# Kernel optimization log

Measured on AMD Instinct MI355X. Metric: run time of the kernel, lower is better.

## Reference

```python
import jax, jax.numpy as jnp
import numpy as np

N_CLASSES = 512


def setup_inputs() -> dict:
    key = jax.random.key(0)
    k1, k2 = jax.random.split(key)
    x0 = jax.random.normal(k1, (16, 8192, 1, 128), dtype=jnp.float32)
    # nn.Parameter(torch.randn(n_channels, n_classes, vec_len) * 0.001)
    embedding0 = jax.random.normal(k2, (1, N_CLASSES, 128), dtype=jnp.float32) * 0.001
    return {"x0": x0, "embedding0": embedding0}


def reference(x0, embedding0):
    # normalize=False path: x = x0, embedding = embedding0
    x = x0
    embedding = embedding0
    B, S, C, L = x.shape
    K = embedding.shape[1]
    xf = x.reshape(B * S, C, L)

    x2 = jnp.sum(xf * xf, axis=-1)                      # (BS, C)
    e2 = jnp.sum(embedding * embedding, axis=-1)        # (C, K)
    dot = jnp.einsum('bcl,ckl->bck', xf, embedding)     # (BS, C, K)
    d2 = x2[:, :, None] - 2.0 * dot + e2[None]          # (BS, C, K)
    index = jnp.argmin(d2, axis=2)                      # (BS, C)

    # entropy of code usage histogram (divided by BS, as in the torch code)
    hist = jnp.zeros((K,), dtype=jnp.float32).at[index.reshape(-1)].add(1.0)
    prob = hist / jnp.float32(index.shape[0])
    entropy = -jnp.sum(jnp.where(prob > 0, prob * jnp.log(jnp.where(prob > 0, prob, 1.0)), 0.0))

    # gather selected codebook vectors: (BS, C, L) -> (B, S, C, L)
    output = embedding[jnp.arange(C)[None, :], index].reshape(B, S, C, L)

    sg = jax.lax.stop_gradient
    out0 = sg(output - x) + x                                   # straight-through
    out1 = jnp.sum((sg(x) - output) ** 2, axis=-1)              # (B, S, C)
    out2 = jnp.sum((x - sg(output)) ** 2, axis=-1) + jnp.sum((x - x0) ** 2, axis=-1)
    return out0, out1, out2, entropy
```

## Files before the change

kernel.cpp:

```cpp
#include <hip/hip_runtime.h>
#include <hip/hip_bf16.h>
#include <math.h>

#define NROWS 131072
#define NCODE 512
#define DIM 128
#define ESCALE 256.0f
#define DESCALE 0.0078125f

typedef long long llong;
typedef __attribute__((ext_vector_type(16))) float f32x16;

__device__ inline llong mk_ll(int lo, int hi) {
    return ((llong)(unsigned long long)(unsigned)hi << 32) | (unsigned)lo;
}

__global__ __launch_bounds__(256) void prep_pack8(const float* __restrict__ emb,
        int4* __restrict__ afp, float* __restrict__ e2p) {
    __shared__ float part[32][8];
    const int tid = threadIdx.x;
    const int mt = blockIdx.x;
    const int lane = tid & 63, q = tid >> 6;
    const int c5 = lane & 31, g = lane >> 5;
    const int code = mt * 32 + c5;
    const float* src = emb + (size_t)code * DIM;

    int w[4];
    float ss = 0.f;
    #pragma unroll
    for (int h = 0; h < 2; ++h) {
        int d0 = (2 * q + h) * 16 + g * 8;
        float4 v0 = *reinterpret_cast<const float4*>(src + d0);
        float4 v1 = *reinterpret_cast<const float4*>(src + d0 + 4);
        ss = fmaf(v0.x, v0.x, ss); ss = fmaf(v0.y, v0.y, ss);
        ss = fmaf(v0.z, v0.z, ss); ss = fmaf(v0.w, v0.w, ss);
        ss = fmaf(v1.x, v1.x, ss); ss = fmaf(v1.y, v1.y, ss);
        ss = fmaf(v1.z, v1.z, ss); ss = fmaf(v1.w, v1.w, ss);
        int lo = __builtin_amdgcn_cvt_pk_fp8_f32(v0.x * ESCALE, v0.y * ESCALE, 0, false);
        lo = __builtin_amdgcn_cvt_pk_fp8_f32(v0.z * ESCALE, v0.w * ESCALE, lo, true);
        int hi = __builtin_amdgcn_cvt_pk_fp8_f32(v1.x * ESCALE, v1.y * ESCALE, 0, false);
        hi = __builtin_amdgcn_cvt_pk_fp8_f32(v1.z * ESCALE, v1.w * ESCALE, hi, true);
        w[2 * h] = lo; w[2 * h + 1] = hi;
    }
    afp[(mt * 4 + q) * 64 + lane] = make_int4(w[0], w[1], w[2], w[3]);
    part[c5][q * 2 + g] = ss;
    __syncthreads();
    if (tid < 32) {
        float s = 0.f;
        #pragma unroll
        for (int j = 0; j < 8; ++j) s += part[tid][j];
        int g2 = (tid >> 2) & 1;
        int r = (tid & 3) | ((tid >> 3) << 2);
        e2p[mt * 32 + g2 * 16 + r] = s;
    }
}

__global__ __launch_bounds__(256, 8) void vq_argmin(
        const float* __restrict__ x, const float* __restrict__ emb,
        const int4* __restrict__ afp, const float* __restrict__ e2p,
        int* __restrict__ idxg,
        float* __restrict__ out0, float* __restrict__ out1, float* __restrict__ out2) {
    __shared__ unsigned char xs8[64][DIM];
    __shared__ float x2s[64];
    __shared__ float s_m[2][2][32];
    __shared__ int   s_i[2][2][32];
    __shared__ int   s_fidx[2][32];

    const int tid = threadIdx.x;
    const int lane = tid & 63, l31 = lane & 31, g = lane >> 5;
    const long row0 = (long)blockIdx.x * 64;

    {
        const float4* xg = reinterpret_cast<const float4*>(x + row0 * DIM);
        #pragma unroll
        for (int it = 0; it < 8; ++it) {
            float4 v = xg[it * 256 + tid];
            int r = it * 8 + (tid >> 5), c = tid & 31;
            float s = v.x * v.x + v.y * v.y + v.z * v.z + v.w * v.w;
            s += __shfl_xor(s, 1);  s += __shfl_xor(s, 2);
            s += __shfl_xor(s, 4);  s += __shfl_xor(s, 8);
            s += __shfl_xor(s, 16);
            if ((tid & 31) == 0) x2s[r] = s;
            int w = __builtin_amdgcn_cvt_pk_fp8_f32(v.x, v.y, 0, false);
            w = __builtin_amdgcn_cvt_pk_fp8_f32(v.z, v.w, w, true);
            int off = (c * 4) ^ ((r & 15) << 3);
            *reinterpret_cast<int*>(&xs8[r][off]) = w;
        }
    }
    __syncthreads();

    const int wv = tid >> 6, rg = wv >> 1, ch = wv & 1;
    const int rr = rg * 32 + l31;

    #define RB(K) *reinterpret_cast<const llong*>(&xs8[rr][((K) * 16 + g * 8) ^ ((rr & 15) << 3)])
    const llong b0 = RB(0), b1 = RB(1), b2 = RB(2), b3 = RB(3);
    const llong b4 = RB(4), b5 = RB(5), b6 = RB(6), b7 = RB(7);
    #undef RB

    float m1 = 1e30f;
    int i1 = 0;

    #pragma unroll 1
    for (int t = 0; t < 8; ++t) {
        const int mt = ch * 8 + t;
        const int4* ap = afp + mt * 256 + lane;
        int4 A0 = ap[0];
        int4 A1 = ap[64];
        int4 A2 = ap[128];
        int4 A3 = ap[192];
        f32x16 acc = {};
        acc = __builtin_amdgcn_mfma_f32_32x32x16_fp8_fp8(mk_ll(A0.x, A0.y), b0, acc, 0, 0, 0);
        acc = __builtin_amdgcn_mfma_f32_32x32x16_fp8_fp8(mk_ll(A0.z, A0.w), b1, acc, 0, 0, 0);
        acc = __builtin_amdgcn_mfma_f32_32x32x16_fp8_fp8(mk_ll(A1.x, A1.y), b2, acc, 0, 0, 0);
        acc = __builtin_amdgcn_mfma_f32_32x32x16_fp8_fp8(mk_ll(A1.z, A1.w), b3, acc, 0, 0, 0);
        acc = __builtin_amdgcn_mfma_f32_32x32x16_fp8_fp8(mk_ll(A2.x, A2.y), b4, acc, 0, 0, 0);
        acc = __builtin_amdgcn_mfma_f32_32x32x16_fp8_fp8(mk_ll(A2.z, A2.w), b5, acc, 0, 0, 0);
        acc = __builtin_amdgcn_mfma_f32_32x32x16_fp8_fp8(mk_ll(A3.x, A3.y), b6, acc, 0, 0, 0);
        acc = __builtin_amdgcn_mfma_f32_32x32x16_fp8_fp8(mk_ll(A3.z, A3.w), b7, acc, 0, 0, 0);

        const float4* ev = reinterpret_cast<const float4*>(e2p + mt * 32 + g * 16);
        const int base = mt * 32 + 4 * g;
        float4 ea = ev[0], eb = ev[1];
        float e8a[8] = {ea.x, ea.y, ea.z, ea.w, eb.x, eb.y, eb.z, eb.w};
        #pragma unroll
        for (int r = 0; r < 8; ++r) {
            float sv = e8a[r] - DESCALE * acc[r];
            int code = base + (r & 3) + 8 * (r >> 2);
            if (sv < m1) { m1 = sv; i1 = code; }
        }
        float4 ec = ev[2], ed = ev[3];
        float e8b[8] = {ec.x, ec.y, ec.z, ec.w, ed.x, ed.y, ed.z, ed.w};
        #pragma unroll
        for (int r = 0; r < 8; ++r) {
            float sv = e8b[r] - DESCALE * acc[8 + r];
            int code = base + 16 + (r & 3) + 8 * (r >> 2);
            if (sv < m1) { m1 = sv; i1 = code; }
        }
    }

    {
        float pm = __shfl_xor(m1, 32);
        int   pi = __shfl_xor(i1, 32);
        if (pm < m1 || (pm == m1 && pi < i1)) { m1 = pm; i1 = pi; }
    }
    if (lane < 32) { s_m[rg][ch][l31] = m1; s_i[rg][ch][l31] = i1; }
    __syncthreads();

    if (ch == 0 && lane < 32) {
        float m1f = s_m[rg][0][l31]; int i1f = s_i[rg][0][l31];
        float pm = s_m[rg][1][l31]; int pi = s_i[rg][1][l31];
        if (pm < m1f || (pm == m1f && pi < i1f)) { m1f = pm; i1f = pi; }
        long row = row0 + rr;
        idxg[row] = i1f;
        s_fidx[rg][l31] = i1f;
        float o = x2s[rr] + m1f;
        out1[row] = o;
        out2[row] = o;
    }
    __syncthreads();

    {
        const float4* e4 = reinterpret_cast<const float4*>(emb);
        float4* o4 = reinterpret_cast<float4*>(out0);
        const int rb = rg * 32 + ch * 16;
        #pragma unroll 4
        for (int rx = 0; rx < 16; rx += 2) {
            int lr = rb + rx + g;
            int c = s_fidx[rg][ch * 16 + rx + g];
            o4[(row0 + lr) * 32 + l31] = e4[c * 32 + l31];
        }
    }
}

__global__ __launch_bounds__(256) void hist_part(const int* __restrict__ idxg,
        int* __restrict__ partial) {
    __shared__ int h[NCODE];
    const int tid = threadIdx.x, b = blockIdx.x;
    h[tid] = 0; h[tid + 256] = 0;
    __syncthreads();
    const int4* i4 = reinterpret_cast<const int4*>(idxg + b * 2048);
    #pragma unroll
    for (int k = 0; k < 2; ++k) {
        int4 v = i4[k * 256 + tid];
        atomicAdd(&h[v.x], 1); atomicAdd(&h[v.y], 1);
        atomicAdd(&h[v.z], 1); atomicAdd(&h[v.w], 1);
    }
    __syncthreads();
    partial[b * NCODE + tid] = h[tid];
    partial[b * NCODE + 256 + tid] = h[tid + 256];
}

__global__ void entropy_kernel(const int* __restrict__ partial,
        float* __restrict__ oent) {
    __shared__ float red[8];
    int tid = threadIdx.x;
    int c = 0;
    #pragma unroll
    for (int b = 0; b < 64; ++b) c += partial[b * NCODE + tid];
    float p = (float)c * (1.0f / 131072.0f);
    float t = (p > 0.f) ? (-p * logf(p)) : 0.f;
    #pragma unroll
    for (int off = 32; off > 0; off >>= 1) t += __shfl_down(t, off);
    if ((tid & 63) == 0) red[tid >> 6] = t;
    __syncthreads();
    if (tid == 0) {
        float s = 0.f;
        #pragma unroll
        for (int i = 0; i < 8; ++i) s += red[i];
        *oent = s;
    }
}

extern "C" void kernel_launch(void* const* d_in, const int* in_sizes, int n_in,
                              void* d_out, int out_size, void* d_ws, size_t ws_size,
                              hipStream_t stream) {
    const float* x   = (const float*)d_in[0];
    const float* emb = (const float*)d_in[1];
    float* out  = (float*)d_out;
    float* out0 = out;
    float* out1 = out0 + (size_t)NROWS * DIM;
    float* out2 = out1 + NROWS;
    float* oent = out2 + NROWS;

    float* e2p = (float*)d_ws;
    int4*  afp = (int4*)((char*)d_ws + 4096);
    int*   idxg = (int*)((char*)d_ws + 4096 + 65536);
    int*   partial = (int*)((char*)d_ws + 4096 + 65536 + 524288);

    prep_pack8<<<16, 256, 0, stream>>>(emb, afp, e2p);
    vq_argmin<<<NROWS / 64, 256, 0, stream>>>(x, emb, afp, e2p, idxg, out0, out1, out2);
    hist_part<<<64, 256, 0, stream>>>(idxg, partial);
    entropy_kernel<<<1, NCODE, 0, stream>>>(partial, oent);
}
```

Before: 53.71 us.

## Process 128 rows per block so each wave reuses codebook fragments twice

```diff
diff --git a/kernel.cpp b/kernel.cpp
--- a/kernel.cpp
+++ b/kernel.cpp
@@ -55,25 +55,25 @@
     }
 }
 
-__global__ __launch_bounds__(256, 8) void vq_argmin(
+__global__ __launch_bounds__(256, 4) void vq_argmin(
         const float* __restrict__ x, const float* __restrict__ emb,
         const int4* __restrict__ afp, const float* __restrict__ e2p,
         int* __restrict__ idxg,
         float* __restrict__ out0, float* __restrict__ out1, float* __restrict__ out2) {
-    __shared__ unsigned char xs8[64][DIM];
-    __shared__ float x2s[64];
-    __shared__ float s_m[2][2][32];
-    __shared__ int   s_i[2][2][32];
-    __shared__ int   s_fidx[2][32];
+    __shared__ unsigned char xs8[128][DIM];
+    __shared__ float x2s[128];
+    __shared__ float s_m[2][2][64];
+    __shared__ int   s_i[2][2][64];
+    __shared__ int   s_fidx[2][64];
 
     const int tid = threadIdx.x;
     const int lane = tid & 63, l31 = lane & 31, g = lane >> 5;
-    const long row0 = (long)blockIdx.x * 64;
+    const long row0 = (long)blockIdx.x * 128;
 
     {
         const float4* xg = reinterpret_cast<const float4*>(x + row0 * DIM);
         #pragma unroll
-        for (int it = 0; it < 8; ++it) {
+        for (int it = 0; it < 16; ++it) {
             float4 v = xg[it * 256 + tid];
             int r = it * 8 + (tid >> 5), c = tid & 31;
             float s = v.x * v.x + v.y * v.y + v.z * v.z + v.w * v.w;
@@ -90,15 +90,18 @@
     __syncthreads();
 
     const int wv = tid >> 6, rg = wv >> 1, ch = wv & 1;
-    const int rr = rg * 32 + l31;
-
-    #define RB(K) *reinterpret_cast<const llong*>(&xs8[rr][((K) * 16 + g * 8) ^ ((rr & 15) << 3)])
-    const llong b0 = RB(0), b1 = RB(1), b2 = RB(2), b3 = RB(3);
-    const llong b4 = RB(4), b5 = RB(5), b6 = RB(6), b7 = RB(7);
+    const int r0 = rg * 64 + l31;
+    const int r1 = rg * 64 + 32 + l31;
+
+    #define RB(RR, K) *reinterpret_cast<const llong*>(&xs8[RR][((K) * 16 + g * 8) ^ (((RR) & 15) << 3)])
+    const llong b0 = RB(r0, 0), b1 = RB(r0, 1), b2 = RB(r0, 2), b3 = RB(r0, 3);
+    const llong b4 = RB(r0, 4), b5 = RB(r0, 5), b6 = RB(r0, 6), b7 = RB(r0, 7);
+    const llong c0 = RB(r1, 0), c1 = RB(r1, 1), c2 = RB(r1, 2), c3 = RB(r1, 3);
+    const llong c4 = RB(r1, 4), c5 = RB(r1, 5), c6 = RB(r1, 6), c7 = RB(r1, 7);
     #undef RB
 
-    float m1 = 1e30f;
-    int i1 = 0;
+    float m1a = 1e30f, m1b = 1e30f;
+    int i1a = 0, i1b = 0;
 
     #pragma unroll 1
     for (int t = 0; t < 8; ++t) {
@@ -108,52 +111,62 @@
         int4 A1 = ap[64];
         int4 A2 = ap[128];
         int4 A3 = ap[192];
-        f32x16 acc = {};
-        acc = __builtin_amdgcn_mfma_f32_32x32x16_fp8_fp8(mk_ll(A0.x, A0.y), b0, acc, 0, 0, 0);
-        acc = __builtin_amdgcn_mfma_f32_32x32x16_fp8_fp8(mk_ll(A0.z, A0.w), b1, acc, 0, 0, 0);
-        acc = __builtin_amdgcn_mfma_f32_32x32x16_fp8_fp8(mk_ll(A1.x, A1.y), b2, acc, 0, 0, 0);
-        acc = __builtin_amdgcn_mfma_f32_32x32x16_fp8_fp8(mk_ll(A1.z, A1.w), b3, acc, 0, 0, 0);
-        acc = __builtin_amdgcn_mfma_f32_32x32x16_fp8_fp8(mk_ll(A2.x, A2.y), b4, acc, 0, 0, 0);
-        acc = __builtin_amdgcn_mfma_f32_32x32x16_fp8_fp8(mk_ll(A2.z, A2.w), b5, acc, 0, 0, 0);
-        acc = __builtin_amdgcn_mfma_f32_32x32x16_fp8_fp8(mk_ll(A3.x, A3.y), b6, acc, 0, 0, 0);
-        acc = __builtin_amdgcn_mfma_f32_32x32x16_fp8_fp8(mk_ll(A3.z, A3.w), b7, acc, 0, 0, 0);
+        f32x16 acc0 = {}, acc1 = {};
+        acc0 = __builtin_amdgcn_mfma_f32_32x32x16_fp8_fp8(mk_ll(A0.x, A0.y), b0, acc0, 0, 0, 0);
+        acc1 = __builtin_amdgcn_mfma_f32_32x32x16_fp8_fp8(mk_ll(A0.x, A0.y), c0, acc1, 0, 0, 0);
+        acc0 = __builtin_amdgcn_mfma_f32_32x32x16_fp8_fp8(mk_ll(A0.z, A0.w), b1, acc0, 0, 0, 0);
+        acc1 = __builtin_amdgcn_mfma_f32_32x32x16_fp8_fp8(mk_ll(A0.z, A0.w), c1, acc1, 0, 0, 0);
+        acc0 = __builtin_amdgcn_mfma_f32_32x32x16_fp8_fp8(mk_ll(A1.x, A1.y), b2, acc0, 0, 0, 0);
+        acc1 = __builtin_amdgcn_mfma_f32_32x32x16_fp8_fp8(mk_ll(A1.x, A1.y), c2, acc1, 0, 0, 0);
+        acc0 = __builtin_amdgcn_mfma_f32_32x32x16_fp8_fp8(mk_ll(A1.z, A1.w), b3, acc0, 0, 0, 0);
+        acc1 = __builtin_amdgcn_mfma_f32_32x32x16_fp8_fp8(mk_ll(A1.z, A1.w), c3, acc1, 0, 0, 0);
+        acc0 = __builtin_amdgcn_mfma_f32_32x32x16_fp8_fp8(mk_ll(A2.x, A2.y), b4, acc0, 0, 0, 0);
+        acc1 = __builtin_amdgcn_mfma_f32_32x32x16_fp8_fp8(mk_ll(A2.x, A2.y), c4, acc1, 0, 0, 0);
+        acc0 = __builtin_amdgcn_mfma_f32_32x32x16_fp8_fp8(mk_ll(A2.z, A2.w), b5, acc0, 0, 0, 0);
+        acc1 = __builtin_amdgcn_mfma_f32_32x32x16_fp8_fp8(mk_ll(A2.z, A2.w), c5, acc1, 0, 0, 0);
+        acc0 = __builtin_amdgcn_mfma_f32_32x32x16_fp8_fp8(mk_ll(A3.x, A3.y), b6, acc0, 0, 0, 0);
+        acc1 = __builtin_amdgcn_mfma_f32_32x32x16_fp8_fp8(mk_ll(A3.x, A3.y), c6, acc1, 0, 0, 0);
+        acc0 = __builtin_amdgcn_mfma_f32_32x32x16_fp8_fp8(mk_ll(A3.z, A3.w), b7, acc0, 0, 0, 0);
+        acc1 = __builtin_amdgcn_mfma_f32_32x32x16_fp8_fp8(mk_ll(A3.z, A3.w), c7, acc1, 0, 0, 0);
 
         const float4* ev = reinterpret_cast<const float4*>(e2p + mt * 32 + g * 16);
         const int base = mt * 32 + 4 * g;
-        float4 ea = ev[0], eb = ev[1];
-        float e8a[8] = {ea.x, ea.y, ea.z, ea.w, eb.x, eb.y, eb.z, eb.w};
-        #pragma unroll
-        for (int r = 0; r < 8; ++r) {
-            float sv = e8a[r] - DESCALE * acc[r];
+        float4 ea = ev[0], eb = ev[1], ec = ev[2], ed = ev[3];
+        float earr[16] = {ea.x, ea.y, ea.z, ea.w, eb.x, eb.y, eb.z, eb.w,
+                          ec.x, ec.y, ec.z, ec.w, ed.x, ed.y, ed.z, ed.w};
+        #pragma unroll
+        for (int r = 0; r < 16; ++r) {
             int code = base + (r & 3) + 8 * (r >> 2);
-            if (sv < m1) { m1 = sv; i1 = code; }
+            float sv0 = earr[r] - DESCALE * acc0[r];
+            float sv1 = earr[r] - DESCALE * acc1[r];
+            if (sv0 < m1a) { m1a = sv0; i1a = code; }
+            if (sv1 < m1b) { m1b = sv1; i1b = code; }
         }
-        float4 ec = ev[2], ed = ev[3];
-        float e8b[8] = {ec.x, ec.y, ec.z, ec.w, ed.x, ed.y, ed.z, ed.w};
-        #pragma unroll
-        for (int r = 0; r < 8; ++r) {
-            float sv = e8b[r] - DESCALE * acc[8 + r];
-            int code = base + 16 + (r & 3) + 8 * (r >> 2);
-            if (sv < m1) { m1 = sv; i1 = code; }
-        }
     }
 
     {
-        float pm = __shfl_xor(m1, 32);
-        int   pi = __shfl_xor(i1, 32);
-        if (pm < m1 || (pm == m1 && pi < i1)) { m1 = pm; i1 = pi; }
-    }
-    if (lane < 32) { s_m[rg][ch][l31] = m1; s_i[rg][ch][l31] = i1; }
-    __syncthreads();
-
-    if (ch == 0 && lane < 32) {
-        float m1f = s_m[rg][0][l31]; int i1f = s_i[rg][0][l31];
-        float pm = s_m[rg][1][l31]; int pi = s_i[rg][1][l31];
+        float pm = __shfl_xor(m1a, 32);
+        int   pi = __shfl_xor(i1a, 32);
+        if (pm < m1a || (pm == m1a && pi < i1a)) { m1a = pm; i1a = pi; }
+        pm = __shfl_xor(m1b, 32);
+        pi = __shfl_xor(i1b, 32);
+        if (pm < m1b || (pm == m1b && pi < i1b)) { m1b = pm; i1b = pi; }
+    }
+    if (lane < 32) {
+        s_m[rg][ch][l31] = m1a;      s_i[rg][ch][l31] = i1a;
+        s_m[rg][ch][32 + l31] = m1b; s_i[rg][ch][32 + l31] = i1b;
+    }
+    __syncthreads();
+
+    if (tid < 128) {
+        int rgx = tid >> 6, lr = tid & 63;
+        float m1f = s_m[rgx][0][lr]; int i1f = s_i[rgx][0][lr];
+        float pm = s_m[rgx][1][lr]; int pi = s_i[rgx][1][lr];
         if (pm < m1f || (pm == m1f && pi < i1f)) { m1f = pm; i1f = pi; }
-        long row = row0 + rr;
+        long row = row0 + tid;
         idxg[row] = i1f;
-        s_fidx[rg][l31] = i1f;
-        float o = x2s[rr] + m1f;
+        s_fidx[rgx][lr] = i1f;
+        float o = x2s[tid] + m1f;
         out1[row] = o;
         out2[row] = o;
     }
@@ -162,11 +175,11 @@
     {
         const float4* e4 = reinterpret_cast<const float4*>(emb);
         float4* o4 = reinterpret_cast<float4*>(out0);
-        const int rb = rg * 32 + ch * 16;
+        const int rb = wv * 32;
         #pragma unroll 4
-        for (int rx = 0; rx < 16; rx += 2) {
+        for (int rx = 0; rx < 32; rx += 2) {
             int lr = rb + rx + g;
-            int c = s_fidx[rg][ch * 16 + rx + g];
+            int c = s_fidx[lr >> 6][lr & 63];
             o4[(row0 + lr) * 32 + l31] = e4[c * 32 + l31];
         }
     }
@@ -228,7 +241,7 @@
     int*   partial = (int*)((char*)d_ws + 4096 + 65536 + 524288);
 
     prep_pack8<<<16, 256, 0, stream>>>(emb, afp, e2p);
-    vq_argmin<<<NROWS / 64, 256, 0, stream>>>(x, emb, afp, e2p, idxg, out0, out1, out2);
+    vq_argmin<<<NROWS / 128, 256, 0, stream>>>(x, emb, afp, e2p, idxg, out0, out1, out2);
     hist_part<<<64, 256, 0, stream>>>(idxg, partial);
     entropy_kernel<<<1, NCODE, 0, stream>>>(partial, oent);
 }
```

Result: faster. 48.54 us (-9.6%).

## Stage codebook in LDS, one wave per 32 rows, pack index into min key

Applied to the files above, without the earlier changes.

```diff
diff --git a/kernel.cpp b/kernel.cpp
--- a/kernel.cpp
+++ b/kernel.cpp
@@ -13,6 +13,10 @@
 
 __device__ inline llong mk_ll(int lo, int hi) {
     return ((llong)(unsigned long long)(unsigned)hi << 32) | (unsigned)lo;
+}
+
+__device__ inline float kstuff(float sv, int code) {
+    return __uint_as_float((__float_as_uint(sv) & 0xFFFFFE00u) | (unsigned)code);
 }
 
 __global__ __launch_bounds__(256) void prep_pack8(const float* __restrict__ emb,
@@ -55,27 +59,27 @@
     }
 }
 
-__global__ __launch_bounds__(256, 8) void vq_argmin(
+__global__ __launch_bounds__(512, 2) void vq_argmin(
         const float* __restrict__ x, const float* __restrict__ emb,
         const int4* __restrict__ afp, const float* __restrict__ e2p,
         int* __restrict__ idxg,
         float* __restrict__ out0, float* __restrict__ out1, float* __restrict__ out2) {
-    __shared__ unsigned char xs8[64][DIM];
-    __shared__ float x2s[64];
-    __shared__ float s_m[2][2][32];
-    __shared__ int   s_i[2][2][32];
-    __shared__ int   s_fidx[2][32];
+    __shared__ unsigned char xs8[256][DIM];
+    __shared__ int4 afp_lds[4096];
+    __shared__ float x2s[256];
 
     const int tid = threadIdx.x;
     const int lane = tid & 63, l31 = lane & 31, g = lane >> 5;
-    const long row0 = (long)blockIdx.x * 64;
+    const int wv = tid >> 6;
+    const long row0 = (long)blockIdx.x * 256;
 
     {
         const float4* xg = reinterpret_cast<const float4*>(x + row0 * DIM);
         #pragma unroll
-        for (int it = 0; it < 8; ++it) {
-            float4 v = xg[it * 256 + tid];
-            int r = it * 8 + (tid >> 5), c = tid & 31;
+        for (int it = 0; it < 16; ++it) {
+            int i = it * 512 + tid;
+            float4 v = xg[i];
+            int r = i >> 5, c = i & 31;
             float s = v.x * v.x + v.y * v.y + v.z * v.z + v.w * v.w;
             s += __shfl_xor(s, 1);  s += __shfl_xor(s, 2);
             s += __shfl_xor(s, 4);  s += __shfl_xor(s, 8);
@@ -87,10 +91,14 @@
             *reinterpret_cast<int*>(&xs8[r][off]) = w;
         }
     }
-    __syncthreads();
-
-    const int wv = tid >> 6, rg = wv >> 1, ch = wv & 1;
-    const int rr = rg * 32 + l31;
+    #pragma unroll
+    for (int it = 0; it < 8; ++it) {
+        int i = it * 512 + tid;
+        afp_lds[i] = afp[i];
+    }
+    __syncthreads();
+
+    const int rr = wv * 32 + l31;
 
     #define RB(K) *reinterpret_cast<const llong*>(&xs8[rr][((K) * 16 + g * 8) ^ ((rr & 15) << 3)])
     const llong b0 = RB(0), b1 = RB(1), b2 = RB(2), b3 = RB(3);
@@ -98,12 +106,10 @@
     #undef RB
 
     float m1 = 1e30f;
-    int i1 = 0;
 
     #pragma unroll 1
-    for (int t = 0; t < 8; ++t) {
-        const int mt = ch * 8 + t;
-        const int4* ap = afp + mt * 256 + lane;
+    for (int mt = 0; mt < 16; ++mt) {
+        const int4* ap = afp_lds + mt * 256 + lane;
         int4 A0 = ap[0];
         int4 A1 = ap[64];
         int4 A2 = ap[128];
@@ -120,54 +126,46 @@
 
         const float4* ev = reinterpret_cast<const float4*>(e2p + mt * 32 + g * 16);
         const int base = mt * 32 + 4 * g;
-        float4 ea = ev[0], eb = ev[1];
-        float e8a[8] = {ea.x, ea.y, ea.z, ea.w, eb.x, eb.y, eb.z, eb.w};
-        #pragma unroll
-        for (int r = 0; r < 8; ++r) {
-            float sv = e8a[r] - DESCALE * acc[r];
+        float4 ea = ev[0], eb = ev[1], ec = ev[2], ed = ev[3];
+        float earr[16] = {ea.x, ea.y, ea.z, ea.w, eb.x, eb.y, eb.z, eb.w,
+                          ec.x, ec.y, ec.z, ec.w, ed.x, ed.y, ed.z, ed.w};
+        float k0[16];
+        #pragma unroll
+        for (int r = 0; r < 16; ++r) {
             int code = base + (r & 3) + 8 * (r >> 2);
-            if (sv < m1) { m1 = sv; i1 = code; }
+            k0[r] = kstuff(earr[r] - DESCALE * acc[r], code);
         }
-        float4 ec = ev[2], ed = ev[3];
-        float e8b[8] = {ec.x, ec.y, ec.z, ec.w, ed.x, ed.y, ed.z, ed.w};
-        #pragma unroll
-        for (int r = 0; r < 8; ++r) {
-            float sv = e8b[r] - DESCALE * acc[8 + r];
-            int code = base + 16 + (r & 3) + 8 * (r >> 2);
-            if (sv < m1) { m1 = sv; i1 = code; }
-        }
-    }
-
-    {
-        float pm = __shfl_xor(m1, 32);
-        int   pi = __shfl_xor(i1, 32);
-        if (pm < m1 || (pm == m1 && pi < i1)) { m1 = pm; i1 = pi; }
-    }
-    if (lane < 32) { s_m[rg][ch][l31] = m1; s_i[rg][ch][l31] = i1; }
-    __syncthreads();
-
-    if (ch == 0 && lane < 32) {
-        float m1f = s_m[rg][0][l31]; int i1f = s_i[rg][0][l31];
-        float pm = s_m[rg][1][l31]; int pi = s_i[rg][1][l31];
-        if (pm < m1f || (pm == m1f && pi < i1f)) { m1f = pm; i1f = pi; }
+        #pragma unroll
+        for (int s = 8; s > 0; s >>= 1)
+            #pragma unroll
+            for (int r = 0; r < s; ++r)
+                k0[r] = fminf(k0[r], k0[r + s]);
+        m1 = fminf(m1, k0[0]);
+    }
+
+    m1 = fminf(m1, __shfl_xor(m1, 32));
+    const unsigned kb = __float_as_uint(m1);
+    const int idx = (int)(kb & 0x1FFu);
+    const float sv = __uint_as_float(kb & 0xFFFFFE00u);
+
+    if (lane < 32) {
         long row = row0 + rr;
-        idxg[row] = i1f;
-        s_fidx[rg][l31] = i1f;
-        float o = x2s[rr] + m1f;
+        idxg[row] = idx;
+        float o = x2s[rr] + sv;
         out1[row] = o;
         out2[row] = o;
     }
-    __syncthreads();
 
     {
         const float4* e4 = reinterpret_cast<const float4*>(emb);
-        float4* o4 = reinterpret_cast<float4*>(out0);
-        const int rb = rg * 32 + ch * 16;
+        float4* o4 = reinterpret_cast<float4*>(out0) + (row0 + wv * 32) * 32;
         #pragma unroll 4
-        for (int rx = 0; rx < 16; rx += 2) {
-            int lr = rb + rx + g;
-            int c = s_fidx[rg][ch * 16 + rx + g];
-            o4[(row0 + lr) * 32 + l31] = e4[c * 32 + l31];
+        for (int rx = 0; rx < 32; rx += 2) {
+            int c0 = __shfl(idx, rx);
+            int c1 = __shfl(idx, rx + 1);
+            int c = g ? c1 : c0;
+            int r = rx + g;
+            o4[r * 32 + l31] = e4[c * 32 + l31];
         }
     }
 }
@@ -228,7 +226,7 @@
     int*   partial = (int*)((char*)d_ws + 4096 + 65536 + 524288);
 
     prep_pack8<<<16, 256, 0, stream>>>(emb, afp, e2p);
-    vq_argmin<<<NROWS / 64, 256, 0, stream>>>(x, emb, afp, e2p, idxg, out0, out1, out2);
+    vq_argmin<<<NROWS / 256, 512, 0, stream>>>(x, emb, afp, e2p, idxg, out0, out1, out2);
     hist_part<<<64, 256, 0, stream>>>(idxg, partial);
     entropy_kernel<<<1, NCODE, 0, stream>>>(partial, oent);
 }
```

After: 62.02 us. 1.15x slower.
